# Kernel tuning notes

Hardware: AMD Instinct MI355X
Metric: run time of the kernel (lower is better)

The kernel has to match this reference:

```python
import jax, jax.numpy as jnp
import numpy as np

EPS = 1.0 / 137.0
NUM_HEADS = 16


def yat_dense(x, kernel, bias, alpha):
    y = jnp.einsum('btc,cf->btf', x, kernel)
    x2 = jnp.sum(x * x, axis=-1, keepdims=True)          # [B,T,1]
    k2 = jnp.sum(kernel * kernel, axis=0)                 # [F]
    y = (y * y) / (x2 + k2 - 2.0 * y + EPS)
    out_f = kernel.shape[1]
    scale = (jnp.sqrt(jnp.float32(out_f)) / jnp.log1p(jnp.float32(out_f))) ** alpha
    return y * scale + bias


def setup_inputs() -> dict:
    key = jax.random.key(0)
    ks = jax.random.split(key, 6)
    B, T, C = 2, 1024, 1024
    x = jax.random.normal(ks[0], (B, T, C), dtype=jnp.float32)
    mask = jnp.tril(jnp.ones((T, T), dtype=bool))[None, None, :, :]  # causal [1,1,T,T]
    w_qkv = jax.random.normal(ks[1], (C, 3 * C), dtype=jnp.float32) * 0.02
    b_qkv = jnp.zeros((3 * C,), dtype=jnp.float32)
    alpha_qkv = jnp.ones((1,), dtype=jnp.float32)
    w_proj = jax.random.normal(ks[2], (C, C), dtype=jnp.float32) * 0.02
    b_proj = jnp.zeros((C,), dtype=jnp.float32)
    alpha_proj = jnp.ones((1,), dtype=jnp.float32)
    alpha_attn = jnp.ones((1,), dtype=jnp.float32)
    return {"x": x, "mask": mask, "w_qkv": w_qkv, "b_qkv": b_qkv,
            "alpha_qkv": alpha_qkv, "w_proj": w_proj, "b_proj": b_proj,
            "alpha_proj": alpha_proj, "alpha_attn": alpha_attn}


def reference(x, mask, w_qkv, b_qkv, alpha_qkv, w_proj, b_proj, alpha_proj, alpha_attn):
    B, T, C = x.shape
    head_dim = C // NUM_HEADS
    scale = jnp.log1p(jnp.float32(head_dim))
    inv_scale = (head_dim / scale) ** alpha_attn  # [1]

    qkv = yat_dense(x, w_qkv, b_qkv, alpha_qkv)               # [B,T,3C]
    qkv = qkv.reshape(B, T, 3, NUM_HEADS, head_dim)
    q, k, v = jnp.moveaxis(qkv, 2, 0)                         # each [B,T,H,hd]
    # NOTE: source transposes with (0,3,1,2) -> [B, head_dim, T, H]; reproduced faithfully.
    q = jnp.transpose(q, (0, 3, 1, 2))
    k = jnp.transpose(k, (0, 3, 1, 2))
    v = jnp.transpose(v, (0, 3, 1, 2))

    dot = jnp.einsum('bhid,bhjd->bhij', q, k)                 # [B,hd,T,T]
    sq_dot = dot * dot
    q2 = jnp.sum(q * q, axis=-1, keepdims=True)               # [B,hd,T,1]
    k2 = jnp.sum(k * k, axis=-1, keepdims=True).transpose(0, 1, 3, 2)  # [B,hd,1,T]
    sq_dist = q2 + k2 - 2.0 * dot
    attn = sq_dot / (sq_dist + EPS)
    attn = attn * inv_scale
    attn = jnp.where(mask, attn, jnp.finfo(jnp.float32).min)
    attn = jax.nn.softmax(attn, axis=-1)

    out = jnp.einsum('bhij,bhjd->bhid', attn, v)              # [B,hd,T,H]
    out = out.transpose(0, 2, 1, 3).reshape(B, T, C)
    out = yat_dense(out, w_proj, b_proj, alpha_proj)
    return out
```

## Files before the change

### kernel.cpp

```cpp
#include <hip/hip_runtime.h>
#include <math.h>

#define YAT_EPS (1.0f / 137.0f)


typedef __bf16 bf16x8 __attribute__((ext_vector_type(8)));
typedef float floatx4 __attribute__((ext_vector_type(4)));
typedef unsigned int uintx4 __attribute__((ext_vector_type(4)));

__device__ __forceinline__ float fast_rcp(float x) {
#if __has_builtin(__builtin_amdgcn_rcpf)
    return __builtin_amdgcn_rcpf(x);
#else
    return 1.0f / x;
#endif
}
__device__ __forceinline__ float fast_exp2(float x) {
#if __has_builtin(__builtin_amdgcn_exp2f)
    return __builtin_amdgcn_exp2f(x);
#else
    return exp2f(x);
#endif
}

__device__ __forceinline__ unsigned short f32_bf16(float f) {
    unsigned u = __builtin_bit_cast(unsigned, f);
    u += 0x7fffu + ((u >> 16) & 1u);
    return (unsigned short)(u >> 16);
}
__device__ __forceinline__ float bf16_f32(unsigned short h) {
    unsigned u = ((unsigned)h) << 16;
    return __builtin_bit_cast(float, u);
}

template <bool PERM>
__global__ void convtrans_kernel(
    const float* __restrict__ W, unsigned short* __restrict__ th,
    unsigned short* __restrict__ tl, float* __restrict__ k2, int K, int N)
{
    __shared__ float t[32][33];
    int tx = threadIdx.x, ty = threadIdx.y;
    int n0 = blockIdx.x * 32, k0 = blockIdx.y * 32;
    #pragma unroll
    for (int r = 0; r < 4; ++r)
        t[ty + r * 8][tx] = W[(size_t)(k0 + ty + r * 8) * N + n0 + tx];
    __syncthreads();
    #pragma unroll
    for (int r = 0; r < 4; ++r) {
        int nl = ty + r * 8;
        int nn = n0 + nl;
        int nw = nn;
        if (PERM) {
            nw = (nn & ~1023) | (((nn & 63) >> 3) << 7)
               | (((nn >> 6) & 15) << 3) | (nn & 7);
        }
        float v = t[tx][nl];
        unsigned short h = f32_bf16(v);
        th[(size_t)nw * K + k0 + tx] = h;
        tl[(size_t)nw * K + k0 + tx] = f32_bf16(v - bf16_f32(h));
        float s = v * v;
        #pragma unroll
        for (int m = 16; m > 0; m >>= 1) s += __shfl_xor(s, m, 32);
        if (tx == 0) atomicAdd(&k2[nn], s);
    }
}

__global__ __launch_bounds__(256) void convx_kernel(
    const float* __restrict__ x, unsigned short* __restrict__ hi,
    unsigned short* __restrict__ lo, float* __restrict__ x2x)
{
    __shared__ float red[4];
    const int row = blockIdx.x, tid = threadIdx.x;
    float4 v = *(const float4*)(x + (size_t)row * 1024 + tid * 4);
    float vv[4] = {v.x, v.y, v.z, v.w};
    unsigned short hh[4], ll[4];
    float s = 0.0f;
    #pragma unroll
    for (int e = 0; e < 4; ++e) {
        hh[e] = f32_bf16(vv[e]);
        ll[e] = f32_bf16(vv[e] - bf16_f32(hh[e]));
        s = fmaf(vv[e], vv[e], s);
    }
    *(ushort4*)(hi + (size_t)row * 1024 + tid * 4) =
        make_ushort4(hh[0], hh[1], hh[2], hh[3]);
    *(ushort4*)(lo + (size_t)row * 1024 + tid * 4) =
        make_ushort4(ll[0], ll[1], ll[2], ll[3]);
    #pragma unroll
    for (int off = 32; off > 0; off >>= 1) s += __shfl_down(s, off, 64);
    if ((tid & 63) == 0) red[tid >> 6] = s;
    __syncthreads();
    if (tid == 0) x2x[row] = red[0] + red[1] + red[2] + red[3];
}

template <int BM, int MODE>
__global__ __launch_bounds__(256) void gemm_yat_mfma_kernel(
    const unsigned short* __restrict__ Ah, const unsigned short* __restrict__ Al,
    const unsigned short* __restrict__ Bh, const unsigned short* __restrict__ Bl,
    const float* __restrict__ bias, const float* __restrict__ x2,
    const float* __restrict__ k2, const float* __restrict__ alphap,
    float* __restrict__ out, int N, int K, float scale_base,
    unsigned short* __restrict__ kvu, float* __restrict__ q2k,
    float* __restrict__ k2k)
{
    constexpr int TM = BM / 32;
    constexpr int NI = (BM * 128 + 16384) / 4096;
    __shared__ __align__(16) unsigned short sbuf[BM * 64 + 8192];

    const int tid = threadIdx.x;
    const int w = tid >> 6, l = tid & 63;
    const int lane16 = l & 15, quad = l >> 4;
    const int wm = w & 1, wn = w >> 1;
    const int m0 = blockIdx.y * BM, n0 = blockIdx.x * 128;

    floatx4 acc[TM][4];
    #pragma unroll
    for (int tm = 0; tm < TM; ++tm)
        #pragma unroll
        for (int tn = 0; tn < 4; ++tn)
            acc[tm][tn] = (floatx4){0.f, 0.f, 0.f, 0.f};

    for (int k0 = 0; k0 < K; k0 += 32) {
        __syncthreads();
        #pragma unroll
        for (int i = 0; i < NI; ++i) {
            const int o = (i * 4 + w) * 1024;
            const unsigned short* gp;
            if (o < BM * 128) {
                const unsigned short* g = (o < BM * 64) ? Ah : Al;
                const int oo = (o < BM * 64) ? o : o - BM * 64;
                gp = g + (size_t)(m0 + (oo >> 6) + (l >> 2)) * K + k0 + (l & 3) * 8;
            } else {
                const int ob = o - BM * 128;
                const unsigned short* g = (ob < 8192) ? Bh : Bl;
                const int oo = ob & 8191;
                gp = g + (size_t)(n0 + (oo >> 6) + (l >> 2)) * K + k0 + (l & 3) * 8;
            }
            __builtin_amdgcn_global_load_lds(
                (const __attribute__((address_space(1))) unsigned int*)gp,
                (__attribute__((address_space(3))) unsigned int*)((char*)sbuf + o),
                16, 0, 0);
        }
        __syncthreads();

        bf16x8 afh[TM], afl[TM], bfh[4], bfl[4];
        #pragma unroll
        for (int tm = 0; tm < TM; ++tm) {
            const int base = (wm * (BM / 2) + tm * 16 + lane16) * 32 + quad * 8;
            afh[tm] = *(const bf16x8*)(sbuf + base);
            afl[tm] = *(const bf16x8*)(sbuf + BM * 32 + base);
        }
        #pragma unroll
        for (int tn = 0; tn < 4; ++tn) {
            const int nb = (wn * 64 + tn * 16 + lane16) * 32 + quad * 8;
            bfh[tn] = *(const bf16x8*)(sbuf + BM * 64 + nb);
            bfl[tn] = *(const bf16x8*)(sbuf + BM * 64 + 4096 + nb);
        }
        #pragma unroll
        for (int tm = 0; tm < TM; ++tm)
            #pragma unroll
            for (int tn = 0; tn < 4; ++tn) {
                acc[tm][tn] = __builtin_amdgcn_mfma_f32_16x16x32_bf16(
                    afh[tm], bfh[tn], acc[tm][tn], 0, 0, 0);
                acc[tm][tn] = __builtin_amdgcn_mfma_f32_16x16x32_bf16(
                    afh[tm], bfl[tn], acc[tm][tn], 0, 0, 0);
                acc[tm][tn] = __builtin_amdgcn_mfma_f32_16x16x32_bf16(
                    afl[tm], bfh[tn], acc[tm][tn], 0, 0, 0);
            }
    }

    const float scale = powf(scale_base, alphap[0]);

    if (MODE == 0) {
        #pragma unroll
        for (int tm = 0; tm < TM; ++tm) {
            #pragma unroll
            for (int tn = 0; tn < 4; ++tn) {
                const int n = n0 + wn * 64 + tn * 16 + lane16;
                const float kk = k2[n];
                const float bb = bias[n];
                const int mrow = m0 + wm * (BM / 2) + tm * 16 + quad * 4;
                #pragma unroll
                for (int r = 0; r < 4; ++r) {
                    const float y = acc[tm][tn][r];
                    const float den = x2[mrow + r] + kk - 2.0f * y + YAT_EPS;
                    out[(size_t)(mrow + r) * N + n] =
                        y * y / den * scale + bb;
                }
            }
        }
    } else {
        float* lds = (float*)sbuf;
        const int s_ = n0 >> 10;
        const int dblk = (n0 >> 7) & 7;
        const int b_ = m0 >> 10;
        const int tl = tid >> 3;
        const int ddr = tid & 7;
        const int d_glob = dblk * 8 + ddr;

        #pragma unroll
        for (int half = 0; half < 2; ++half) {
            __syncthreads();
            if (wm == half) {
                #pragma unroll
                for (int tm = 0; tm < TM; ++tm) {
                    #pragma unroll
                    for (int tn = 0; tn < 4; ++tn) {
                        const int n = n0 + wn * 64 + tn * 16 + lane16;
                        const int hcol = (n >> 3) & 15;
                        const int norig = (n & ~1023) | (hcol << 6)
                                        | (dblk << 3) | (n & 7);
                        const float kk = k2[norig];
                        const float bb = bias[norig];
                        const int mrow = m0 + wm * 32 + tm * 16 + quad * 4;
                        const int tbase = tm * 16 + quad * 4;
                        const int col = wn * 64 + tn * 16 + lane16;
                        #pragma unroll
                        for (int r = 0; r < 4; ++r) {
                            const float y = acc[tm][tn][r];
                            const float den =
                                x2[mrow + r] + kk - 2.0f * y + YAT_EPS;
                            lds[(tbase + r) * 132 + col] =
                                y * y / den * scale + bb;
                        }
                    }
                }
            }
            __syncthreads();

            float y[16];
            #pragma unroll
            for (int h = 0; h < 16; ++h)
                y[h] = lds[tl * 132 + h * 8 + ddr];
            const int t_glob = (m0 & 1023) + half * 32 + tl;

            if (s_ < 2) {
                unsigned short hb[16], lb[16];
                float s2 = 0.f;
                #pragma unroll
                for (int h = 0; h < 16; ++h) {
                    hb[h] = f32_bf16(y[h]);
                    lb[h] = f32_bf16(y[h] - bf16_f32(hb[h]));
                    s2 = fmaf(y[h], y[h], s2);
                }
                unsigned short* dst = kvu + (size_t)b_ * 6291456
                    + (s_ == 0 ? 4194304u : 0u)
                    + ((size_t)(d_glob * 1024 + t_glob)) * 32;
                #pragma unroll
                for (int h4 = 0; h4 < 4; ++h4) {
                    *(ushort4*)(dst + h4 * 4) = make_ushort4(
                        hb[h4*4], hb[h4*4+1], hb[h4*4+2], hb[h4*4+3]);
                    *(ushort4*)(dst + 16 + h4 * 4) = make_ushort4(
                        lb[h4*4], lb[h4*4+1], lb[h4*4+2], lb[h4*4+3]);
                }
                float* sq = (s_ == 0) ? q2k : k2k;
                sq[b_ * 65536 + d_glob * 1024 + t_glob] = s2;
            } else {
                const int j = t_glob;
                const int jt2 = j >> 5;
                const int e = ((j >> 4) & 1) * 4 + (j & 3);
                const int qd = (j >> 2) & 3;
                unsigned short* dst = kvu + (size_t)b_ * 6291456 + 2097152
                    + d_glob * 32768 + jt2 * 1024 + qd * 128 + e;
                #pragma unroll
                for (int h = 0; h < 16; ++h) {
                    const unsigned short vh = f32_bf16(y[h]);
                    dst[h * 8] = vh;
                    dst[512 + h * 8] = f32_bf16(y[h] - bf16_f32(vh));
                }
            }
        }
    }
}

__global__ __launch_bounds__(256) void yat_attn_mfma2_kernel(
    const unsigned short* __restrict__ KVU,
    const float* __restrict__ k2k, const float* __restrict__ q2k,
    const float* __restrict__ alphap,
    unsigned short* __restrict__ attn_h, unsigned short* __restrict__ attn_l,
    float* __restrict__ x2a)
{
    const int tid = threadIdx.x;
    const int lane = tid & 63, w = tid >> 6;
    const int lane16 = lane & 15, quad = lane >> 4;
    const int d = blockIdx.x, c = blockIdx.y, b = blockIdx.z;

    const float isc =
        powf(64.0f / log1pf(64.0f), alphap[0]) * 1.44269504f;

    const unsigned short* kp = KVU + (size_t)b * 6291456 + d * 32768;
    const unsigned short* vp = KVU + (size_t)b * 6291456 + 2097152 + d * 32768;
    const unsigned short* qp = KVU + (size_t)b * 6291456 + 4194304 + d * 32768;
    const float* k2bd = k2k + b * 65536 + d * 1024;
    const float* q2bd = q2k + b * 65536 + d * 1024;

    const int ti0 = c * 4 + w;
    const int tiA = ti0, tiB = 63 - ti0;

    const bf16x8 qA = *(const bf16x8*)(qp + (tiA * 16 + lane16) * 32 + quad * 8);
    const bf16x8 qB = *(const bf16x8*)(qp + (tiB * 16 + lane16) * 32 + quad * 8);
    const float q2A = q2bd[tiA * 16 + lane16] + YAT_EPS;
    const float q2B = q2bd[tiB * 16 + lane16] + YAT_EPS;
    const int iA = tiA * 16 + lane16;
    const int iB = tiB * 16 + lane16;

    floatx4 OA = (floatx4){0.f, 0.f, 0.f, 0.f};
    floatx4 OB = (floatx4){0.f, 0.f, 0.f, 0.f};
    float lsA = 0.f, lsB = 0.f;

    const int lastA = tiA >> 1, lastB = tiB >> 1;

    for (int jt2 = 0; jt2 <= lastB; ++jt2) {
        const int j0 = jt2 * 32;
        const unsigned short* kp0 = kp + (j0 + lane16) * 32;
        const unsigned short* kp1 = kp + (j0 + 16 + lane16) * 32;
        const bf16x8 k0a = *(const bf16x8*)(kp0 + quad * 8);
        const bf16x8 k0b = *(const bf16x8*)(kp0 + ((quad ^ 2) * 8));
        const bf16x8 k1a = *(const bf16x8*)(kp1 + quad * 8);
        const bf16x8 k1b = *(const bf16x8*)(kp1 + ((quad ^ 2) * 8));
        const unsigned short* vpj = vp + jt2 * 1024 + quad * 128 + lane16 * 8;
        const bf16x8 vh = *(const bf16x8*)(vpj);
        const bf16x8 vl = *(const bf16x8*)(vpj + 512);
        const float4 k20 = *(const float4*)(k2bd + j0 + quad * 4);
        const float4 k21 = *(const float4*)(k2bd + j0 + 16 + quad * 4);
        const float k2r[8] = {k20.x, k20.y, k20.z, k20.w,
                              k21.x, k21.y, k21.z, k21.w};
        const int jbase0 = j0 + quad * 4;

        #pragma unroll
        for (int half = 0; half < 2; ++half) {
            if (half == 0 && jt2 > lastA) continue;
            const bf16x8 qf = half ? qB : qA;
            const float q2e = half ? q2B : q2A;
            const int iM = half ? iB : iA;
            floatx4 S0 = __builtin_amdgcn_mfma_f32_16x16x32_bf16(
                k0a, qf, (floatx4){0.f, 0.f, 0.f, 0.f}, 0, 0, 0);
            S0 = __builtin_amdgcn_mfma_f32_16x16x32_bf16(k0b, qf, S0, 0, 0, 0);
            floatx4 S1 = __builtin_amdgcn_mfma_f32_16x16x32_bf16(
                k1a, qf, (floatx4){0.f, 0.f, 0.f, 0.f}, 0, 0, 0);
            S1 = __builtin_amdgcn_mfma_f32_16x16x32_bf16(k1b, qf, S1, 0, 0, 0);

            float p[8], lsum = 0.f;
            #pragma unroll
            for (int e = 0; e < 8; ++e) {
                const float s = (e < 4) ? S0[e & 3] : S1[e & 3];
                const int j = jbase0 + (e >> 2) * 16 + (e & 3);
                const float den = fmaf(-2.f, s, q2e + k2r[e]);
                float pe = fast_exp2(s * s * fast_rcp(den) * isc);
                pe = (j <= iM) ? pe : 0.f;
                lsum += pe;
                p[e] = pe;
            }
            if (half) lsB += lsum; else lsA += lsum;

            unsigned ph32[4], pl32[4];
            #pragma unroll
            for (int e2 = 0; e2 < 4; ++e2) {
                const unsigned b0 = __builtin_bit_cast(unsigned, p[e2 * 2]);
                const unsigned b1 = __builtin_bit_cast(unsigned, p[e2 * 2 + 1]);
                const unsigned r0 = b0 + 0x7fffu + ((b0 >> 16) & 1u);
                const unsigned r1 = b1 + 0x7fffu + ((b1 >> 16) & 1u);
                ph32[e2] = (r0 >> 16) | (r1 & 0xFFFF0000u);
                const float f0 = p[e2 * 2] -
                    __builtin_bit_cast(float, r0 & 0xFFFF0000u);
                const float f1 = p[e2 * 2 + 1] -
                    __builtin_bit_cast(float, r1 & 0xFFFF0000u);
                pl32[e2] = (__builtin_bit_cast(unsigned, f0) >> 16) |
                           (__builtin_bit_cast(unsigned, f1) & 0xFFFF0000u);
            }
            const bf16x8 Ph = __builtin_bit_cast(bf16x8,
                (uintx4){ph32[0], ph32[1], ph32[2], ph32[3]});
            const bf16x8 Pl = __builtin_bit_cast(bf16x8,
                (uintx4){pl32[0], pl32[1], pl32[2], pl32[3]});

            floatx4 O = half ? OB : OA;
            O = __builtin_amdgcn_mfma_f32_16x16x32_bf16(Ph, vh, O, 0, 0, 0);
            O = __builtin_amdgcn_mfma_f32_16x16x32_bf16(Pl, vh, O, 0, 0, 0);
            O = __builtin_amdgcn_mfma_f32_16x16x32_bf16(Ph, vl, O, 0, 0, 0);
            if (half) OB = O; else OA = O;
        }
    }

    #pragma unroll
    for (int half = 0; half < 2; ++half) {
        float ls = half ? lsB : lsA;
        const floatx4 O = half ? OB : OA;
        const int ti = half ? tiB : tiA;
        ls += __shfl_xor(ls, 16, 64);
        ls += __shfl_xor(ls, 32, 64);
        const float linv = 1.0f / ls;
        #pragma unroll
        for (int r = 0; r < 4; ++r) {
            const float lr = __shfl(linv, quad * 4 + r, 16);
            const float v = O[r] * lr;
            const int i = ti * 16 + quad * 4 + r;
            const size_t off =
                ((size_t)(b * 1024 + i)) * 1024 + d * 16 + lane16;
            const unsigned short vh16 = f32_bf16(v);
            attn_h[off] = vh16;
            attn_l[off] = f32_bf16(v - bf16_f32(vh16));
            float s2 = v * v;
            s2 += __shfl_xor(s2, 1, 64);
            s2 += __shfl_xor(s2, 2, 64);
            s2 += __shfl_xor(s2, 4, 64);
            s2 += __shfl_xor(s2, 8, 64);
            if (lane16 == 0) atomicAdd(&x2a[b * 1024 + i], s2);
        }
    }
}

extern "C" void kernel_launch(void* const* d_in, const int* in_sizes, int n_in,
                              void* d_out, int out_size, void* d_ws, size_t ws_size,
                              hipStream_t stream)
{
    const float* x          = (const float*)d_in[0];
    const float* w_qkv      = (const float*)d_in[2];
    const float* b_qkv      = (const float*)d_in[3];
    const float* alpha_qkv  = (const float*)d_in[4];
    const float* w_proj     = (const float*)d_in[5];
    const float* b_proj     = (const float*)d_in[6];
    const float* alpha_proj = (const float*)d_in[7];
    const float* alpha_attn = (const float*)d_in[8];
    float* out = (float*)d_out;

    float* ws = (float*)d_ws;
    unsigned short* KVU  = (unsigned short*)ws;
    unsigned short* WtQh = (unsigned short*)(ws + 6291456);
    unsigned short* WtQl = (unsigned short*)(ws + 7864320);
    unsigned short* WtPh = (unsigned short*)(ws + 9437184);
    unsigned short* WtPl = (unsigned short*)(ws + 9961472);
    unsigned short* xh   = (unsigned short*)(ws + 10485760);
    unsigned short* xl   = (unsigned short*)(ws + 11534336);
    float* x2x  = ws + 12582912;
    float* x2a  = ws + 12584960;
    float* k2q  = ws + 12587008;
    float* k2p  = ws + 12590080;
    float* k2k  = ws + 12591104;
    float* q2k  = ws + 12722176;
    unsigned short* attn_h = WtQh;
    unsigned short* attn_l = WtQl;

    hipMemsetAsync(x2a, 0, (2048 + 3072 + 1024) * sizeof(float), stream);

    convtrans_kernel<true><<<dim3(96, 32), dim3(32, 8), 0, stream>>>(
        w_qkv, WtQh, WtQl, k2q, 1024, 3072);
    convtrans_kernel<false><<<dim3(32, 32), dim3(32, 8), 0, stream>>>(
        w_proj, WtPh, WtPl, k2p, 1024, 1024);
    convx_kernel<<<2048, 256, 0, stream>>>(x, xh, xl, x2x);

    const float sb_qkv = sqrtf(3072.0f) / log1pf(3072.0f);
    gemm_yat_mfma_kernel<64, 2><<<dim3(24, 32), 256, 0, stream>>>(
        xh, xl, WtQh, WtQl, b_qkv, x2x, k2q, alpha_qkv, nullptr,
        3072, 1024, sb_qkv, KVU, q2k, k2k);

    yat_attn_mfma2_kernel<<<dim3(64, 8, 2), 256, 0, stream>>>(
        KVU, k2k, q2k, alpha_attn, attn_h, attn_l, x2a);

    const float sb_proj = sqrtf(1024.0f) / log1pf(1024.0f);
    gemm_yat_mfma_kernel<64, 0><<<dim3(8, 32), 256, 0, stream>>>(
        attn_h, attn_l, WtPh, WtPl, b_proj, x2a, k2p, alpha_proj, out,
        1024, 1024, sb_proj, nullptr, nullptr, nullptr);
}
```

Baseline: 252.2 us.

## Merge prep kernels, shrink proj GEMM tile, truncate P split in attention

Three weight/input conversion kernels are merged into one launch, cutting launch overhead. The GEMM gets a BN template parameter, and the output projection uses 64-wide N tiles, doubling its grid to 512 blocks for better CU occupancy. The attention kernel now splits P into hi/lo bf16 by truncation rather than round-to-nearest, saving ALU ops. The lo part still captures the residual, so accuracy should hold.

```diff
diff --git a/kernel.cpp b/kernel.cpp
--- a/kernel.cpp
+++ b/kernel.cpp
@@ -33,66 +33,80 @@
     return __builtin_bit_cast(float, u);
 }
 
-template <bool PERM>
-__global__ void convtrans_kernel(
-    const float* __restrict__ W, unsigned short* __restrict__ th,
-    unsigned short* __restrict__ tl, float* __restrict__ k2, int K, int N)
+__global__ __launch_bounds__(256) void prep_kernel(
+    const float* __restrict__ x,
+    const float* __restrict__ w_qkv, const float* __restrict__ w_proj,
+    unsigned short* __restrict__ xh, unsigned short* __restrict__ xl,
+    float* __restrict__ x2x,
+    unsigned short* __restrict__ WtQh, unsigned short* __restrict__ WtQl,
+    float* __restrict__ k2q,
+    unsigned short* __restrict__ WtPh, unsigned short* __restrict__ WtPl,
+    float* __restrict__ k2p)
 {
     __shared__ float t[32][33];
-    int tx = threadIdx.x, ty = threadIdx.y;
-    int n0 = blockIdx.x * 32, k0 = blockIdx.y * 32;
-    #pragma unroll
-    for (int r = 0; r < 4; ++r)
-        t[ty + r * 8][tx] = W[(size_t)(k0 + ty + r * 8) * N + n0 + tx];
-    __syncthreads();
-    #pragma unroll
-    for (int r = 0; r < 4; ++r) {
-        int nl = ty + r * 8;
-        int nn = n0 + nl;
-        int nw = nn;
-        if (PERM) {
-            nw = (nn & ~1023) | (((nn & 63) >> 3) << 7)
-               | (((nn >> 6) & 15) << 3) | (nn & 7);
-        }
-        float v = t[tx][nl];
-        unsigned short h = f32_bf16(v);
-        th[(size_t)nw * K + k0 + tx] = h;
-        tl[(size_t)nw * K + k0 + tx] = f32_bf16(v - bf16_f32(h));
-        float s = v * v;
-        #pragma unroll
-        for (int m = 16; m > 0; m >>= 1) s += __shfl_xor(s, m, 32);
-        if (tx == 0) atomicAdd(&k2[nn], s);
+    const int bid = blockIdx.x;
+    const int tid = threadIdx.x;
+
+    if (bid < 4096) {
+        const bool isQ = bid < 3072;
+        const float* W = isQ ? w_qkv : w_proj;
+        unsigned short* th = isQ ? WtQh : WtPh;
+        unsigned short* tl = isQ ? WtQl : WtPl;
+        float* k2 = isQ ? k2q : k2p;
+        const int N = isQ ? 3072 : 1024;
+        const int id2 = isQ ? bid : bid - 3072;
+        const int nx = isQ ? (id2 % 96) : (id2 & 31);
+        const int ky = isQ ? (id2 / 96) : (id2 >> 5);
+        const int tx = tid & 31, ty = tid >> 5;
+        const int n0 = nx * 32, k0 = ky * 32;
+        #pragma unroll
+        for (int r = 0; r < 4; ++r)
+            t[ty + r * 8][tx] = W[(size_t)(k0 + ty + r * 8) * N + n0 + tx];
+        __syncthreads();
+        #pragma unroll
+        for (int r = 0; r < 4; ++r) {
+            const int nl = ty + r * 8;
+            const int nn = n0 + nl;
+            int nw = nn;
+            if (isQ) {
+                nw = (nn & ~1023) | (((nn & 63) >> 3) << 7)
+                   | (((nn >> 6) & 15) << 3) | (nn & 7);
+            }
+            const float v = t[tx][nl];
+            const unsigned short h = f32_bf16(v);
+            th[(size_t)nw * 1024 + k0 + tx] = h;
+            tl[(size_t)nw * 1024 + k0 + tx] = f32_bf16(v - bf16_f32(h));
+            float s = v * v;
+            #pragma unroll
+            for (int m = 16; m > 0; m >>= 1) s += __shfl_xor(s, m, 32);
+            if (tx == 0) atomicAdd(&k2[nn], s);
+        }
+    } else {
+        const int row = bid - 4096;
+        float* red = &t[0][0];
+        float4 v = *(const float4*)(x + (size_t)row * 1024 + tid * 4);
+        float vv[4] = {v.x, v.y, v.z, v.w};
+        unsigned short hh[4], ll[4];
+        float s = 0.0f;
+        #pragma unroll
+        for (int e = 0; e < 4; ++e) {
+            hh[e] = f32_bf16(vv[e]);
+            ll[e] = f32_bf16(vv[e] - bf16_f32(hh[e]));
+            s = fmaf(vv[e], vv[e], s);
+        }
+        *(ushort4*)(xh + (size_t)row * 1024 + tid * 4) =
+            make_ushort4(hh[0], hh[1], hh[2], hh[3]);
+        *(ushort4*)(xl + (size_t)row * 1024 + tid * 4) =
+            make_ushort4(ll[0], ll[1], ll[2], ll[3]);
+        #pragma unroll
+        for (int off = 32; off > 0; off >>= 1) s += __shfl_down(s, off, 64);
+        if ((tid & 63) == 0) red[tid >> 6] = s;
+        __syncthreads();
+        if (tid == 0) x2x[row] = red[0] + red[1] + red[2] + red[3];
     }
 }
 
-__global__ __launch_bounds__(256) void convx_kernel(
-    const float* __restrict__ x, unsigned short* __restrict__ hi,
-    unsigned short* __restrict__ lo, float* __restrict__ x2x)
-{
-    __shared__ float red[4];
-    const int row = blockIdx.x, tid = threadIdx.x;
-    float4 v = *(const float4*)(x + (size_t)row * 1024 + tid * 4);
-    float vv[4] = {v.x, v.y, v.z, v.w};
-    unsigned short hh[4], ll[4];
-    float s = 0.0f;
-    #pragma unroll
-    for (int e = 0; e < 4; ++e) {
-        hh[e] = f32_bf16(vv[e]);
-        ll[e] = f32_bf16(vv[e] - bf16_f32(hh[e]));
-        s = fmaf(vv[e], vv[e], s);
-    }
-    *(ushort4*)(hi + (size_t)row * 1024 + tid * 4) =
-        make_ushort4(hh[0], hh[1], hh[2], hh[3]);
-    *(ushort4*)(lo + (size_t)row * 1024 + tid * 4) =
-        make_ushort4(ll[0], ll[1], ll[2], ll[3]);
-    #pragma unroll
-    for (int off = 32; off > 0; off >>= 1) s += __shfl_down(s, off, 64);
-    if ((tid & 63) == 0) red[tid >> 6] = s;
-    __syncthreads();
-    if (tid == 0) x2x[row] = red[0] + red[1] + red[2] + red[3];
-}
-
-template <int BM, int MODE>
+template <int BM, int BN, int MODE>
 __global__ __launch_bounds__(256) void gemm_yat_mfma_kernel(
     const unsigned short* __restrict__ Ah, const unsigned short* __restrict__ Al,
     const unsigned short* __restrict__ Bh, const unsigned short* __restrict__ Bl,
@@ -103,20 +117,21 @@
     float* __restrict__ k2k)
 {
     constexpr int TM = BM / 32;
-    constexpr int NI = (BM * 128 + 16384) / 4096;
-    __shared__ __align__(16) unsigned short sbuf[BM * 64 + 8192];
+    constexpr int TN = BN / 32;
+    constexpr int NI = (BM + BN) / 32;
+    __shared__ __align__(16) unsigned short sbuf[BM * 64 + BN * 64];
 
     const int tid = threadIdx.x;
     const int w = tid >> 6, l = tid & 63;
     const int lane16 = l & 15, quad = l >> 4;
     const int wm = w & 1, wn = w >> 1;
-    const int m0 = blockIdx.y * BM, n0 = blockIdx.x * 128;
-
-    floatx4 acc[TM][4];
+    const int m0 = blockIdx.y * BM, n0 = blockIdx.x * BN;
+
+    floatx4 acc[TM][TN];
     #pragma unroll
     for (int tm = 0; tm < TM; ++tm)
         #pragma unroll
-        for (int tn = 0; tn < 4; ++tn)
+        for (int tn = 0; tn < TN; ++tn)
             acc[tm][tn] = (floatx4){0.f, 0.f, 0.f, 0.f};
 
     for (int k0 = 0; k0 < K; k0 += 32) {
@@ -127,12 +142,12 @@
             const unsigned short* gp;
             if (o < BM * 128) {
                 const unsigned short* g = (o < BM * 64) ? Ah : Al;
-                const int oo = (o < BM * 64) ? o : o - BM * 64;
+                const int oo = o & (BM * 64 - 1);
                 gp = g + (size_t)(m0 + (oo >> 6) + (l >> 2)) * K + k0 + (l & 3) * 8;
             } else {
                 const int ob = o - BM * 128;
-                const unsigned short* g = (ob < 8192) ? Bh : Bl;
-                const int oo = ob & 8191;
+                const unsigned short* g = (ob < BN * 64) ? Bh : Bl;
+                const int oo = ob & (BN * 64 - 1);
                 gp = g + (size_t)(n0 + (oo >> 6) + (l >> 2)) * K + k0 + (l & 3) * 8;
             }
             __builtin_amdgcn_global_load_lds(
@@ -142,7 +157,7 @@
         }
         __syncthreads();
 
-        bf16x8 afh[TM], afl[TM], bfh[4], bfl[4];
+        bf16x8 afh[TM], afl[TM], bfh[TN], bfl[TN];
         #pragma unroll
         for (int tm = 0; tm < TM; ++tm) {
             const int base = (wm * (BM / 2) + tm * 16 + lane16) * 32 + quad * 8;
@@ -150,15 +165,15 @@
             afl[tm] = *(const bf16x8*)(sbuf + BM * 32 + base);
         }
         #pragma unroll
-        for (int tn = 0; tn < 4; ++tn) {
-            const int nb = (wn * 64 + tn * 16 + lane16) * 32 + quad * 8;
+        for (int tn = 0; tn < TN; ++tn) {
+            const int nb = (wn * (BN / 2) + tn * 16 + lane16) * 32 + quad * 8;
             bfh[tn] = *(const bf16x8*)(sbuf + BM * 64 + nb);
-            bfl[tn] = *(const bf16x8*)(sbuf + BM * 64 + 4096 + nb);
+            bfl[tn] = *(const bf16x8*)(sbuf + BM * 64 + BN * 32 + nb);
         }
         #pragma unroll
         for (int tm = 0; tm < TM; ++tm)
             #pragma unroll
-            for (int tn = 0; tn < 4; ++tn) {
+            for (int tn = 0; tn < TN; ++tn) {
                 acc[tm][tn] = __builtin_amdgcn_mfma_f32_16x16x32_bf16(
                     afh[tm], bfh[tn], acc[tm][tn], 0, 0, 0);
                 acc[tm][tn] = __builtin_amdgcn_mfma_f32_16x16x32_bf16(
@@ -174,8 +189,8 @@
         #pragma unroll
         for (int tm = 0; tm < TM; ++tm) {
             #pragma unroll
-            for (int tn = 0; tn < 4; ++tn) {
-                const int n = n0 + wn * 64 + tn * 16 + lane16;
+            for (int tn = 0; tn < TN; ++tn) {
+                const int n = n0 + wn * (BN / 2) + tn * 16 + lane16;
                 const float kk = k2[n];
                 const float bb = bias[n];
                 const int mrow = m0 + wm * (BM / 2) + tm * 16 + quad * 4;
@@ -204,8 +219,8 @@
                 #pragma unroll
                 for (int tm = 0; tm < TM; ++tm) {
                     #pragma unroll
-                    for (int tn = 0; tn < 4; ++tn) {
-                        const int n = n0 + wn * 64 + tn * 16 + lane16;
+                    for (int tn = 0; tn < TN; ++tn) {
+                        const int n = n0 + wn * (BN / 2) + tn * 16 + lane16;
                         const int hcol = (n >> 3) & 15;
                         const int norig = (n & ~1023) | (hcol << 6)
                                         | (dblk << 3) | (n & 7);
@@ -213,7 +228,7 @@
                         const float bb = bias[norig];
                         const int mrow = m0 + wm * 32 + tm * 16 + quad * 4;
                         const int tbase = tm * 16 + quad * 4;
-                        const int col = wn * 64 + tn * 16 + lane16;
+                        const int col = wn * (BN / 2) + tn * 16 + lane16;
                         #pragma unroll
                         for (int r = 0; r < 4; ++r) {
                             const float y = acc[tm][tn][r];
@@ -357,13 +372,11 @@
             for (int e2 = 0; e2 < 4; ++e2) {
                 const unsigned b0 = __builtin_bit_cast(unsigned, p[e2 * 2]);
                 const unsigned b1 = __builtin_bit_cast(unsigned, p[e2 * 2 + 1]);
-                const unsigned r0 = b0 + 0x7fffu + ((b0 >> 16) & 1u);
-                const unsigned r1 = b1 + 0x7fffu + ((b1 >> 16) & 1u);
-                ph32[e2] = (r0 >> 16) | (r1 & 0xFFFF0000u);
+                ph32[e2] = (b0 >> 16) | (b1 & 0xFFFF0000u);
                 const float f0 = p[e2 * 2] -
-                    __builtin_bit_cast(float, r0 & 0xFFFF0000u);
+                    __builtin_bit_cast(float, b0 & 0xFFFF0000u);
                 const float f1 = p[e2 * 2 + 1] -
-                    __builtin_bit_cast(float, r1 & 0xFFFF0000u);
+                    __builtin_bit_cast(float, b1 & 0xFFFF0000u);
                 pl32[e2] = (__builtin_bit_cast(unsigned, f0) >> 16) |
                            (__builtin_bit_cast(unsigned, f1) & 0xFFFF0000u);
             }
@@ -441,14 +454,11 @@
 
     hipMemsetAsync(x2a, 0, (2048 + 3072 + 1024) * sizeof(float), stream);
 
-    convtrans_kernel<true><<<dim3(96, 32), dim3(32, 8), 0, stream>>>(
-        w_qkv, WtQh, WtQl, k2q, 1024, 3072);
-    convtrans_kernel<false><<<dim3(32, 32), dim3(32, 8), 0, stream>>>(
-        w_proj, WtPh, WtPl, k2p, 1024, 1024);
-    convx_kernel<<<2048, 256, 0, stream>>>(x, xh, xl, x2x);
+    prep_kernel<<<6144, 256, 0, stream>>>(
+        x, w_qkv, w_proj, xh, xl, x2x, WtQh, WtQl, k2q, WtPh, WtPl, k2p);
 
     const float sb_qkv = sqrtf(3072.0f) / log1pf(3072.0f);
-    gemm_yat_mfma_kernel<64, 2><<<dim3(24, 32), 256, 0, stream>>>(
+    gemm_yat_mfma_kernel<64, 128, 2><<<dim3(24, 32), 256, 0, stream>>>(
         xh, xl, WtQh, WtQl, b_qkv, x2x, k2q, alpha_qkv, nullptr,
         3072, 1024, sb_qkv, KVU, q2k, k2k);
 
@@ -456,7 +466,7 @@
         KVU, k2k, q2k, alpha_attn, attn_h, attn_l, x2a);
 
     const float sb_proj = sqrtf(1024.0f) / log1pf(1024.0f);
-    gemm_yat_mfma_kernel<64, 0><<<dim3(8, 32), 256, 0, stream>>>(
+    gemm_yat_mfma_kernel<64, 64, 0><<<dim3(16, 32), 256, 0, stream>>>(
         attn_h, attn_l, WtPh, WtPl, b_proj, x2a, k2p, alpha_proj, out,
         1024, 1024, sb_proj, nullptr, nullptr, nullptr);
 }
```

After: 230.1 us. 8.7% less time.
